# Kernel optimization log

Hardware: AMD Instinct MI355X
Metric: run time of the kernel (lower is better)

The kernel has to match this reference:

```python
import jax, jax.numpy as jnp
import numpy as np

N, E, D, ED = 50000, 800000, 64, 2


def setup_inputs() -> dict:
    key = jax.random.key(0)
    ks = jax.random.split(key, 16)
    inp = {
        "h": jax.random.normal(ks[0], (N, D), jnp.float32),
        "coord": jax.random.normal(ks[1], (N, 3), jnp.float32),
        "edge_index": jax.random.randint(ks[2], (2, E), 0, N, jnp.int32),
        "edge_attr": jax.random.normal(ks[3], (E, ED), jnp.float32),
        # edge_mlp: Linear(2D+1+ED -> D), Linear(D -> D)
        "W_e1": jax.random.normal(ks[4], (2 * D + 1 + ED, D), jnp.float32) * 0.08,
        "b_e1": jnp.zeros((D,), jnp.float32),
        "W_e2": jax.random.normal(ks[5], (D, D), jnp.float32) * 0.12,
        "b_e2": jnp.zeros((D,), jnp.float32),
        # node_mlp: Linear(D+D -> D), Linear(D -> D)
        "W_n1": jax.random.normal(ks[6], (2 * D, D), jnp.float32) * 0.08,
        "b_n1": jnp.zeros((D,), jnp.float32),
        "W_n2": jax.random.normal(ks[7], (D, D), jnp.float32) * 0.12,
        "b_n2": jnp.zeros((D,), jnp.float32),
        # coord_mlp: Linear(D -> D), Linear(D -> 1, bias=False, xavier gain 0.001)
        "W_c1": jax.random.normal(ks[8], (D, D), jnp.float32) * 0.12,
        "b_c1": jnp.zeros((D,), jnp.float32),
        "W_c2": jax.random.normal(ks[9], (D, 1), jnp.float32) * 1e-3,
    }
    return inp


def reference(h, coord, edge_index, edge_attr,
              W_e1, b_e1, W_e2, b_e2,
              W_n1, b_n1, W_n2, b_n2,
              W_c1, b_c1, W_c2):
    row, col = edge_index[0], edge_index[1]
    n_nodes = h.shape[0]

    # coord2radial
    coord_diff = coord[row] - coord[col]                       # [E,3]
    radial = jnp.sum(coord_diff * coord_diff, axis=-1, keepdims=True)  # [E,1]

    # edge_model
    e_in = jnp.concatenate([h[row], h[col], radial, edge_attr], axis=-1)  # [E, 2D+1+ED]
    e = jax.nn.silu(e_in @ W_e1 + b_e1)
    edge_feat = jax.nn.silu(e @ W_e2 + b_e2)                   # [E,D]

    # coord_model: trans = coord_diff * coord_mlp(edge_feat), clamp, segment mean
    scale = jax.nn.silu(edge_feat @ W_c1 + b_c1) @ W_c2        # [E,1]
    trans = jnp.clip(coord_diff * scale, -100.0, 100.0)        # [E,3]
    agg_c = jax.ops.segment_sum(trans, row, num_segments=n_nodes)       # [N,3]
    cnt = jax.ops.segment_sum(jnp.ones((trans.shape[0],), trans.dtype), row,
                              num_segments=n_nodes)            # [N]
    coord_out = coord + agg_c / jnp.clip(cnt, 1.0, None)[:, None]  # coords_weight=1.0

    # node_model: segment sum of edge_feat by row, node MLP, residual
    agg_h = jax.ops.segment_sum(edge_feat, row, num_segments=n_nodes)   # [N,D]
    n_in = jnp.concatenate([h, agg_h], axis=-1)                # [N,2D]
    h_out = h + (jax.nn.silu(n_in @ W_n1 + b_n1) @ W_n2 + b_n2)

    return (h_out, coord_out)
```

## Files before the change

kernel.cpp:

```cpp
#include <hip/hip_runtime.h>

#define DD 64
#define SLOTMAX 64

using s8v   = __attribute__((ext_vector_type(8))) short;
using f32x4 = __attribute__((ext_vector_type(4))) float;

typedef unsigned int   uint_t;
typedef unsigned short ushort_t;

union U8 { s8v v; uint_t u[4]; };

__device__ __forceinline__ float silu_f(float x) {
    return x / (1.0f + __expf(-x));
}
__device__ __forceinline__ float clamp100(float x) {
    return fminf(fmaxf(x, -100.0f), 100.0f);
}
__device__ __forceinline__ unsigned short f2bf(float x) {
    unsigned int u = __float_as_uint(x);
    return (unsigned short)((u + 0x7FFFu + ((u >> 16) & 1u)) >> 16);
}
__device__ __forceinline__ float bf2f(ushort_t v) {
    return __uint_as_float(((uint_t)v) << 16);
}
__device__ __forceinline__ uint_t cvt_pk_bf16(float lo, float hi) {
    uint_t r;
    asm("v_cvt_pk_bf16_f32 %0, %1, %2" : "=v"(r) : "v"(lo), "v"(hi));
    return r;
}

#define WAVE_FENCE() do { asm volatile("s_waitcnt lgkmcnt(0)" ::: "memory"); \
                          __builtin_amdgcn_sched_barrier(0); } while (0)

__global__ __launch_bounds__(256) void prep_all(
    const float* __restrict__ h,
    const float* __restrict__ coord,
    const float* __restrict__ We1, const float* __restrict__ We2,
    const float* __restrict__ Wc1,
    const float* __restrict__ Wn1, const float* __restrict__ Wn2,
    const float* __restrict__ be1, const float* __restrict__ be2,
    const float* __restrict__ bc1,
    const int*   __restrict__ ei,
    ushort_t* __restrict__ hbf,
    ushort_t* __restrict__ wf,
    float4* __restrict__ coord4,
    int* __restrict__ cnt_i,
    int* __restrict__ slots,
    int N, int E, int total8, int histBlocks, int hbfBlocks, int c4Blocks)
{
    const int b = blockIdx.x;
    if (b < histBlocks) {
        const int e = b * 256 + threadIdx.x;
        if (e < E) {
            const int r = ei[e];
            const int s = atomicAdd(&cnt_i[r], 1);
            if (s < SLOTMAX) slots[(size_t)r * SLOTMAX + s] = e;
        }
    } else if (b < histBlocks + hbfBlocks) {
        const int t = (b - histBlocks) * 256 + threadIdx.x;
        if (t < total8) {
            const float4 v0 = ((const float4*)h)[t * 2 + 0];
            const float4 v1 = ((const float4*)h)[t * 2 + 1];
            uint4 o;
            o.x = (uint_t)f2bf(v0.x) | ((uint_t)f2bf(v0.y) << 16);
            o.y = (uint_t)f2bf(v0.z) | ((uint_t)f2bf(v0.w) << 16);
            o.z = (uint_t)f2bf(v1.x) | ((uint_t)f2bf(v1.y) << 16);
            o.w = (uint_t)f2bf(v1.z) | ((uint_t)f2bf(v1.w) << 16);
            ((uint4*)hbf)[t] = o;
        }
    } else if (b < histBlocks + hbfBlocks + c4Blocks) {
        const int t = (b - histBlocks - hbfBlocks) * 256 + threadIdx.x;
        if (t < N) {
            float4 c;
            c.x = coord[3 * t + 0];
            c.y = coord[3 * t + 1];
            c.z = coord[3 * t + 2];
            c.w = 0.0f;
            coord4[t] = c;
        }
    } else {
        const int t = (b - histBlocks - hbfBlocks - c4Blocks) * 256 + threadIdx.x;
        if (t >= 32768) return;
        if (t < 28672) {
            const int j    = t & 7;
            const int lane = (t >> 3) & 63;
            const int n0   = (t >> 9) & 3;
            const int k0   = (t >> 11) & 1;
            const int mat  = t >> 12;
            const int g    = lane >> 4;
            int k;
            if (mat == 2 || mat == 3) k = 16 * (2 * k0 + (j >> 2)) + 4 * g + (j & 3);
            else                      k = k0 * 32 + g * 8 + j;
            const int n = n0 * 16 + (lane & 15);
            float v;
            if      (mat == 0) v = We1[(size_t)k * 64 + n];
            else if (mat == 1) v = We1[(size_t)(64 + k) * 64 + n];
            else if (mat == 2) v = We2[(size_t)k * 64 + n];
            else if (mat == 3) v = Wc1[(size_t)k * 64 + n];
            else if (mat == 4) v = Wn1[(size_t)k * 64 + n];
            else if (mat == 5) v = Wn1[(size_t)(64 + k) * 64 + n];
            else               v = Wn2[(size_t)k * 64 + n];
            wf[t] = f2bf(v);
        } else {
            const int t2   = t - 28672;
            const int j    = t2 & 7;
            const int lane = (t2 >> 3) & 63;
            const int n0   = (t2 >> 9) & 3;
            const int xm   = (t2 >> 11) & 1;
            const int k = 8 * (lane >> 4) + j;
            const int m = n0 * 16 + (lane & 15);
            float v = 0.0f;
            if (xm == 0) {
                if      (k == 0) v = We1[(size_t)128 * 64 + m];
                else if (k == 1) v = We1[(size_t)129 * 64 + m];
                else if (k == 2) v = We1[(size_t)130 * 64 + m];
                else if (k == 3) v = be1[m];
            } else {
                if      (k == 0) v = be2[m];
                else if (k == 1) v = bc1[m];
            }
            wf[t] = f2bf(v);
        }
    }
}

__global__ __launch_bounds__(512, 4) void egcl_edge(
    const ushort_t* __restrict__ hbf,
    const ushort_t* __restrict__ wfG,
    const float4* __restrict__ coord4,
    const int*   __restrict__ ei,
    const float* __restrict__ ea,
    const float* __restrict__ Wc2,
    uint_t* __restrict__ efu,
    float4* __restrict__ trans4,
    int E, int ntiles, int totalWaves)
{
    __shared__ ushort_t fragLDS[20480];

    const int tid = threadIdx.x;
    #pragma unroll
    for (int i = 0; i < 4; ++i)
        ((uint4*)fragLDS)[tid + i * 512] = ((const uint4*)wfG)[tid + i * 512];
    ((uint4*)fragLDS)[2048 + tid] = ((const uint4*)wfG)[3584 + tid];
    __syncthreads();

    const int wid  = tid >> 6;
    const int lane = tid & 63;
    const int l15  = lane & 15;
    const int g    = lane >> 4;

#define LD_W(mat, k0, m0) \
    (*(const s8v*)(fragLDS + ((((mat)*2 + (k0))*4 + (m0)) * 512) + lane * 8))
#define LD_X7(m0) (*(const s8v*)(fragLDS + 16384 + (m0) * 512 + lane * 8))
#define LD_XB(m0) (*(const s8v*)(fragLDS + 18432 + (m0) * 512 + lane * 8))

    float wc2_c[4][4];
    #pragma unroll
    for (int m0 = 0; m0 < 4; ++m0)
        #pragma unroll
        for (int j = 0; j < 4; ++j)
            wc2_c[m0][j] = Wc2[m0 * 16 + 4 * g + j];

    U8 b2f, bcf;
    b2f.u[0] = 0x00003F80u; b2f.u[1] = 0; b2f.u[2] = 0; b2f.u[3] = 0;
    bcf.u[0] = 0x3F800000u; bcf.u[1] = 0; bcf.u[2] = 0; bcf.u[3] = 0;

    const f32x4 zero4 = {0.f, 0.f, 0.f, 0.f};

    for (int t = blockIdx.x * 8 + wid; t < ntiles; t += totalWaves) {
        const int e   = t * 16 + l15;
        const bool val = (e < E);
        const int eL  = val ? e : (E - 1);

        const int row = ei[eL];
        const int col = ei[E + eL];
        const float4 cr = coord4[row];
        const float4 cc = coord4[col];
        const float2 a2 = *(const float2*)(ea + 2 * (size_t)eL);
        const ushort_t* hr = hbf + (size_t)row * 64;
        const ushort_t* hc = hbf + (size_t)col * 64;
        const s8v br0 = *(const s8v*)(hr + g * 8);
        const s8v br1 = *(const s8v*)(hr + 32 + g * 8);
        const s8v bc0 = *(const s8v*)(hc + g * 8);
        const s8v bc1 = *(const s8v*)(hc + 32 + g * 8);

        const float dx = cr.x - cc.x, dy = cr.y - cc.y, dz = cr.z - cc.z;
        const float radial = dx * dx + dy * dy + dz * dz;

        U8 ex;
        ex.u[0] = cvt_pk_bf16(radial, a2.x);
        ex.u[1] = cvt_pk_bf16(a2.y, 1.0f);
        ex.u[2] = 0; ex.u[3] = 0;

        f32x4 c1[4];
        #pragma unroll
        for (int m0 = 0; m0 < 4; ++m0) {
            f32x4 a = zero4;
            a = __builtin_amdgcn_mfma_f32_16x16x32_bf16(LD_W(0, 0, m0), br0, a, 0, 0, 0);
            a = __builtin_amdgcn_mfma_f32_16x16x32_bf16(LD_W(0, 1, m0), br1, a, 0, 0, 0);
            a = __builtin_amdgcn_mfma_f32_16x16x32_bf16(LD_W(1, 0, m0), bc0, a, 0, 0, 0);
            a = __builtin_amdgcn_mfma_f32_16x16x32_bf16(LD_W(1, 1, m0), bc1, a, 0, 0, 0);
            a = __builtin_amdgcn_mfma_f32_16x16x32_bf16(LD_X7(m0),      ex.v, a, 0, 0, 0);
            c1[m0] = a;
        }

        U8 f2a, f2b;
        #pragma unroll
        for (int m0 = 0; m0 < 4; ++m0) {
            const float ya = silu_f(c1[m0][0]);
            const float yb = silu_f(c1[m0][1]);
            const float yc = silu_f(c1[m0][2]);
            const float yd = silu_f(c1[m0][3]);
            U8& dst = (m0 < 2) ? f2a : f2b;
            dst.u[(m0 & 1) * 2 + 0] = cvt_pk_bf16(ya, yb);
            dst.u[(m0 & 1) * 2 + 1] = cvt_pk_bf16(yc, yd);
        }

        f32x4 c2[4];
        #pragma unroll
        for (int m0 = 0; m0 < 4; ++m0) {
            f32x4 a = zero4;
            a = __builtin_amdgcn_mfma_f32_16x16x32_bf16(LD_W(2, 0, m0), f2a.v, a, 0, 0, 0);
            a = __builtin_amdgcn_mfma_f32_16x16x32_bf16(LD_W(2, 1, m0), f2b.v, a, 0, 0, 0);
            a = __builtin_amdgcn_mfma_f32_16x16x32_bf16(LD_XB(m0),      b2f.v, a, 0, 0, 0);
            c2[m0] = a;
        }

        uint_t* efrow = efu + (size_t)e * 32;
        U8 f3a, f3b;
        #pragma unroll
        for (int m0 = 0; m0 < 4; ++m0) {
            const float ya = silu_f(c2[m0][0]);
            const float yb = silu_f(c2[m0][1]);
            const float yc = silu_f(c2[m0][2]);
            const float yd = silu_f(c2[m0][3]);
            const uint_t p0 = cvt_pk_bf16(ya, yb);
            const uint_t p1 = cvt_pk_bf16(yc, yd);
            U8& dst = (m0 < 2) ? f3a : f3b;
            dst.u[(m0 & 1) * 2 + 0] = p0;
            dst.u[(m0 & 1) * 2 + 1] = p1;
            if (val) {
                uint2 st; st.x = p0; st.y = p1;
                *(uint2*)(efrow + m0 * 8 + g * 2) = st;
            }
        }

        float p = 0.f;
        #pragma unroll
        for (int m0 = 0; m0 < 4; ++m0) {
            f32x4 a = zero4;
            a = __builtin_amdgcn_mfma_f32_16x16x32_bf16(LD_W(3, 0, m0), f3a.v, a, 0, 0, 0);
            a = __builtin_amdgcn_mfma_f32_16x16x32_bf16(LD_W(3, 1, m0), f3b.v, a, 0, 0, 0);
            a = __builtin_amdgcn_mfma_f32_16x16x32_bf16(LD_XB(m0),      bcf.v, a, 0, 0, 0);
            #pragma unroll
            for (int j = 0; j < 4; ++j)
                p = fmaf(silu_f(a[j]), wc2_c[m0][j], p);
        }
        p += __shfl_xor(p, 16, 64);
        p += __shfl_xor(p, 32, 64);

        if (val && g == 0) {
            float4 tr;
            tr.x = clamp100(dx * p);
            tr.y = clamp100(dy * p);
            tr.z = clamp100(dz * p);
            tr.w = 1.0f;
            trans4[e] = tr;
        }
    }
#undef LD_W
#undef LD_X7
#undef LD_XB
}

__global__ __launch_bounds__(256) void egcl_agg(
    const ushort_t* __restrict__ efbf,
    const float4* __restrict__ trans4,
    const int* __restrict__ slots,
    const int* __restrict__ cnt_i,
    const float4* __restrict__ coord4,
    ushort_t* __restrict__ aggbf,
    float* __restrict__ coord_out,
    int N)
{
    const int wid  = threadIdx.x >> 6;
    const int lane = threadIdx.x & 63;
    const int n = blockIdx.x * 4 + wid;
    if (n >= N) return;

    const int deg = cnt_i[n];
    const int eff = deg < SLOTMAX ? deg : SLOTMAX;
    const int* sp = slots + (size_t)n * SLOTMAX;

    float a0 = 0.f, a1 = 0.f, a2 = 0.f, a3 = 0.f;
    float tx = 0.f, ty = 0.f, tz = 0.f;

    int s = 0;
    for (; s + 4 <= eff; s += 4) {
        const int e0 = sp[s], e1 = sp[s + 1], e2 = sp[s + 2], e3 = sp[s + 3];
        const float4 t0 = trans4[e0], t1 = trans4[e1], t2 = trans4[e2], t3 = trans4[e3];
        const ushort_t v0 = efbf[(size_t)e0 * 64 + lane];
        const ushort_t v1 = efbf[(size_t)e1 * 64 + lane];
        const ushort_t v2 = efbf[(size_t)e2 * 64 + lane];
        const ushort_t v3 = efbf[(size_t)e3 * 64 + lane];
        a0 += bf2f(v0); a1 += bf2f(v1); a2 += bf2f(v2); a3 += bf2f(v3);
        tx += t0.x + t1.x + t2.x + t3.x;
        ty += t0.y + t1.y + t2.y + t3.y;
        tz += t0.z + t1.z + t2.z + t3.z;
    }
    for (; s < eff; ++s) {
        const int e0 = sp[s];
        a0 += bf2f(efbf[(size_t)e0 * 64 + lane]);
        const float4 t0 = trans4[e0];
        tx += t0.x; ty += t0.y; tz += t0.z;
    }

    aggbf[(size_t)n * 64 + lane] = f2bf(a0 + a1 + a2 + a3);
    if (lane == 0) {
        const float inv = 1.0f / fmaxf((float)deg, 1.0f);
        const float4 cn = coord4[n];
        coord_out[(size_t)n * 3 + 0] = cn.x + tx * inv;
        coord_out[(size_t)n * 3 + 1] = cn.y + ty * inv;
        coord_out[(size_t)n * 3 + 2] = cn.z + tz * inv;
    }
}

__global__ __launch_bounds__(512, 4) void egcl_node(
    const ushort_t* __restrict__ hbf,
    const ushort_t* __restrict__ aggbf,
    const ushort_t* __restrict__ wfG,
    const float* __restrict__ h,
    const float* __restrict__ bn1,
    const float* __restrict__ bn2,
    float* __restrict__ h_out,
    int N)
{
    __shared__ ushort_t fragLDS[12288];
    __shared__ ushort_t ldsY[8][16 * 72];

    const int tid = threadIdx.x;
    #pragma unroll
    for (int i = 0; i < 3; ++i)
        ((uint4*)fragLDS)[tid + i * 512] = ((const uint4*)(wfG + 16384))[tid + i * 512];
    __syncthreads();

    const int wid  = tid >> 6;
    const int lane = tid & 63;
    const int l15  = lane & 15;
    const int g    = lane >> 4;

#define LD_WN(mat, k0, n0) \
    (*(const s8v*)(fragLDS + ((((mat)*2 + (k0))*4 + (n0)) * 512) + lane * 8))

    float bn1_c[4], bn2_c[4];
    #pragma unroll
    for (int n0 = 0; n0 < 4; ++n0) {
        bn1_c[n0] = bn1[n0 * 16 + l15];
        bn2_c[n0] = bn2[n0 * 16 + l15];
    }

    const int wg = blockIdx.x * 8 + wid;
    const int nb = wg * 16;
    if (nb >= N) return;

    const int nod  = nb + l15;
    const int nodL = nod < N ? nod : N - 1;
    const ushort_t* hrow = hbf   + (size_t)nodL * 64;
    const ushort_t* arow = aggbf + (size_t)nodL * 64;
    const s8v aH0 = *(const s8v*)(hrow + g * 8);
    const s8v aH1 = *(const s8v*)(hrow + 32 + g * 8);
    const s8v aG0 = *(const s8v*)(arow + g * 8);
    const s8v aG1 = *(const s8v*)(arow + 32 + g * 8);

    ushort_t* yw = ldsY[wid];
    #pragma unroll
    for (int n0 = 0; n0 < 4; ++n0) {
        f32x4 a = {0.f, 0.f, 0.f, 0.f};
        a = __builtin_amdgcn_mfma_f32_16x16x32_bf16(aH0, LD_WN(0, 0, n0), a, 0, 0, 0);
        a = __builtin_amdgcn_mfma_f32_16x16x32_bf16(aH1, LD_WN(0, 1, n0), a, 0, 0, 0);
        a = __builtin_amdgcn_mfma_f32_16x16x32_bf16(aG0, LD_WN(1, 0, n0), a, 0, 0, 0);
        a = __builtin_amdgcn_mfma_f32_16x16x32_bf16(aG1, LD_WN(1, 1, n0), a, 0, 0, 0);
        #pragma unroll
        for (int jj = 0; jj < 4; ++jj)
            yw[(g * 4 + jj) * 72 + n0 * 16 + l15] = f2bf(silu_f(a[jj] + bn1_c[n0]));
    }
    WAVE_FENCE();

    const ushort_t* yrow = yw + l15 * 72;
    const s8v b0 = *(const s8v*)(yrow + g * 8);
    const s8v b1 = *(const s8v*)(yrow + 32 + g * 8);
    #pragma unroll
    for (int n0 = 0; n0 < 4; ++n0) {
        f32x4 a = {0.f, 0.f, 0.f, 0.f};
        a = __builtin_amdgcn_mfma_f32_16x16x32_bf16(b0, LD_WN(2, 0, n0), a, 0, 0, 0);
        a = __builtin_amdgcn_mfma_f32_16x16x32_bf16(b1, LD_WN(2, 1, n0), a, 0, 0, 0);
        #pragma unroll
        for (int jj = 0; jj < 4; ++jj) {
            const int m = nb + g * 4 + jj;
            if (m < N) {
                const size_t idx = (size_t)m * 64 + n0 * 16 + l15;
                h_out[idx] = h[idx] + (a[jj] + bn2_c[n0]);
            }
        }
    }
#undef LD_WN
}

extern "C" void kernel_launch(void* const* d_in, const int* in_sizes, int n_in,
                              void* d_out, int out_size, void* d_ws, size_t ws_size,
                              hipStream_t stream) {
    const float* h     = (const float*)d_in[0];
    const float* coord = (const float*)d_in[1];
    const int*   ei    = (const int*)  d_in[2];
    const float* ea    = (const float*)d_in[3];
    const float* We1   = (const float*)d_in[4];
    const float* be1   = (const float*)d_in[5];
    const float* We2   = (const float*)d_in[6];
    const float* be2   = (const float*)d_in[7];
    const float* Wn1   = (const float*)d_in[8];
    const float* bn1   = (const float*)d_in[9];
    const float* Wn2   = (const float*)d_in[10];
    const float* bn2   = (const float*)d_in[11];
    const float* Wc1   = (const float*)d_in[12];
    const float* bc1   = (const float*)d_in[13];
    const float* Wc2   = (const float*)d_in[14];

    const int N = in_sizes[0] / DD;
    const int E = in_sizes[3] / 2;

    float* out       = (float*)d_out;
    float* h_out     = out;
    float* coord_out = out + (size_t)N * DD;

    char* base = (char*)d_ws;
    ushort_t* hbf   = (ushort_t*)base;
    const size_t o_wf    = (size_t)N * DD * 2;
    ushort_t* wf    = (ushort_t*)(base + o_wf);
    const size_t o_agg   = o_wf + 32768 * 2;
    ushort_t* aggbf = (ushort_t*)(base + o_agg);
    const size_t o_c4    = o_agg + (size_t)N * DD * 2;
    float4* coord4  = (float4*)(base + o_c4);
    const size_t o_cnt   = o_c4 + (size_t)N * 16;
    int* cnt_i      = (int*)(base + o_cnt);
    const size_t o_slots = o_cnt + (size_t)N * 4;
    int* slots      = (int*)(base + o_slots);
    const size_t o_tr    = o_slots + (size_t)N * SLOTMAX * 4;
    float4* trans4  = (float4*)(base + o_tr);
    const size_t o_ef    = o_tr + (size_t)E * 16;
    ushort_t* efbf  = (ushort_t*)(base + o_ef);

    hipMemsetAsync((void*)cnt_i, 0, (size_t)N * 4, stream);

    const int histBlocks = (E + 255) / 256;
    const int total8     = N * DD / 8;
    const int hbfBlocks  = (total8 + 255) / 256;
    const int c4Blocks   = (N + 255) / 256;
    const int wfBlocks   = (32768 + 255) / 256;
    prep_all<<<histBlocks + hbfBlocks + c4Blocks + wfBlocks, 256, 0, stream>>>(
        h, coord, We1, We2, Wc1, Wn1, Wn2, be1, be2, bc1, ei,
        hbf, wf, coord4, cnt_i, slots, N, E, total8,
        histBlocks, hbfBlocks, c4Blocks);

    const int ntiles = (E + 15) / 16;
    const int eblocks = 1024;
    const int totalWaves = eblocks * 8;
    egcl_edge<<<eblocks, 512, 0, stream>>>(
        hbf, wf, coord4, ei, ea, Wc2,
        (uint_t*)efbf, trans4, E, ntiles, totalWaves);

    const int ablocks = (N + 3) / 4;
    egcl_agg<<<ablocks, 256, 0, stream>>>(
        efbf, trans4, slots, cnt_i, coord4, aggbf, coord_out, N);

    const int nwaves  = (N + 15) / 16;
    const int nblocks = (nwaves + 7) / 8;
    egcl_node<<<nblocks, 512, 0, stream>>>(
        hbf, aggbf, wf, h, bn1, bn2, h_out, N);
}
```

Before: 218.8 us.

## Sort edges by destination row into CSR order so aggregation reads contiguously

Replaces the per-node slot lists with a CSR-style permutation. A scan kernel computes per-node start offsets and a fill kernel writes packed (row, col, bf16 edge_attr) records in row-grouped order. The edge kernel reads these packed records and writes edge features and trans in permuted order, so the aggregation kernel reads each node's edges as contiguous vectorized rows instead of scattered 128-byte gathers. In exchange it adds two extra launches and a second atomic pass over the edges, and block order from the atomic cursor makes the edge order nondeterministic.

After: 227.3 us. +3.9%, slower.

```diff
diff --git a/kernel.cpp b/kernel.cpp
--- a/kernel.cpp
+++ b/kernel.cpp
@@ -46,17 +46,12 @@
     ushort_t* __restrict__ wf,
     float4* __restrict__ coord4,
     int* __restrict__ cnt_i,
-    int* __restrict__ slots,
     int N, int E, int total8, int histBlocks, int hbfBlocks, int c4Blocks)
 {
     const int b = blockIdx.x;
     if (b < histBlocks) {
         const int e = b * 256 + threadIdx.x;
-        if (e < E) {
-            const int r = ei[e];
-            const int s = atomicAdd(&cnt_i[r], 1);
-            if (s < SLOTMAX) slots[(size_t)r * SLOTMAX + s] = e;
-        }
+        if (e < E) atomicAdd(&cnt_i[ei[e]], 1);
     } else if (b < histBlocks + hbfBlocks) {
         const int t = (b - histBlocks) * 256 + threadIdx.x;
         if (t < total8) {
@@ -125,16 +120,62 @@
     }
 }
 
+__global__ __launch_bounds__(256) void prep_scan(
+    const int* __restrict__ cnt_i,
+    int* __restrict__ cursor,
+    int* __restrict__ nstart,
+    int N)
+{
+    __shared__ int sdata[256];
+    __shared__ int sbase;
+    const int tid = threadIdx.x;
+    const int n = blockIdx.x * 256 + tid;
+    int deg = 0;
+    if (n < N) { deg = cnt_i[n]; if (deg > SLOTMAX) deg = SLOTMAX; }
+    sdata[tid] = deg;
+    __syncthreads();
+    for (int off = 1; off < 256; off <<= 1) {
+        const int t = (tid >= off) ? sdata[tid - off] : 0;
+        __syncthreads();
+        sdata[tid] += t;
+        __syncthreads();
+    }
+    if (tid == 255) sbase = atomicAdd(cursor, sdata[255]);
+    __syncthreads();
+    if (n < N) nstart[n] = sbase + sdata[tid] - deg;
+}
+
+__global__ __launch_bounds__(256) void prep_fill(
+    const int* __restrict__ ei,
+    const float* __restrict__ ea,
+    const int* __restrict__ nstart,
+    int* __restrict__ cnt2,
+    int4* __restrict__ eperm4,
+    int E)
+{
+    const int e = blockIdx.x * 256 + threadIdx.x;
+    if (e >= E) return;
+    const int r = ei[e];
+    const int s = atomicAdd(&cnt2[r], 1);
+    if (s < SLOTMAX) {
+        const int c = ei[E + e];
+        const float2 a2 = *(const float2*)(ea + 2 * (size_t)e);
+        const uint_t pk = cvt_pk_bf16(a2.x, a2.y);
+        int4 v; v.x = r; v.y = c; v.z = (int)pk; v.w = 0;
+        eperm4[(size_t)nstart[r] + s] = v;
+    }
+}
+
 __global__ __launch_bounds__(512, 4) void egcl_edge(
     const ushort_t* __restrict__ hbf,
     const ushort_t* __restrict__ wfG,
     const float4* __restrict__ coord4,
-    const int*   __restrict__ ei,
-    const float* __restrict__ ea,
+    const int4* __restrict__ eperm4,
+    const int* __restrict__ cursorP,
     const float* __restrict__ Wc2,
     uint_t* __restrict__ efu,
     float4* __restrict__ trans4,
-    int E, int ntiles, int totalWaves)
+    int totalWaves)
 {
     __shared__ ushort_t fragLDS[20480];
 
@@ -145,6 +186,7 @@
     ((uint4*)fragLDS)[2048 + tid] = ((const uint4*)wfG)[3584 + tid];
     __syncthreads();
 
+    const int P = cursorP[0];
     const int wid  = tid >> 6;
     const int lane = tid & 63;
     const int l15  = lane & 15;
@@ -168,16 +210,18 @@
 
     const f32x4 zero4 = {0.f, 0.f, 0.f, 0.f};
 
-    for (int t = blockIdx.x * 8 + wid; t < ntiles; t += totalWaves) {
-        const int e   = t * 16 + l15;
-        const bool val = (e < E);
-        const int eL  = val ? e : (E - 1);
-
-        const int row = ei[eL];
-        const int col = ei[E + eL];
+    for (int t = blockIdx.x * 8 + wid; t * 16 < P; t += totalWaves) {
+        const int p   = t * 16 + l15;
+        const bool val = (p < P);
+        const int pL  = val ? p : (P - 1);
+
+        const int4 e4 = eperm4[pL];
+        const int row = e4.x;
+        const int col = e4.y;
+        const uint_t eap = (uint_t)e4.z;
+
         const float4 cr = coord4[row];
         const float4 cc = coord4[col];
-        const float2 a2 = *(const float2*)(ea + 2 * (size_t)eL);
         const ushort_t* hr = hbf + (size_t)row * 64;
         const ushort_t* hc = hbf + (size_t)col * 64;
         const s8v br0 = *(const s8v*)(hr + g * 8);
@@ -189,8 +233,9 @@
         const float radial = dx * dx + dy * dy + dz * dz;
 
         U8 ex;
-        ex.u[0] = cvt_pk_bf16(radial, a2.x);
-        ex.u[1] = cvt_pk_bf16(a2.y, 1.0f);
+        const float ea0f = __uint_as_float(eap << 16);
+        ex.u[0] = cvt_pk_bf16(radial, ea0f);
+        ex.u[1] = (eap >> 16) | 0x3F800000u;
         ex.u[2] = 0; ex.u[3] = 0;
 
         f32x4 c1[4];
@@ -227,7 +272,7 @@
             c2[m0] = a;
         }
 
-        uint_t* efrow = efu + (size_t)e * 32;
+        uint_t* efrow = efu + (size_t)pL * 32;
         U8 f3a, f3b;
         #pragma unroll
         for (int m0 = 0; m0 < 4; ++m0) {
@@ -246,7 +291,7 @@
             }
         }
 
-        float p = 0.f;
+        float pacc = 0.f;
         #pragma unroll
         for (int m0 = 0; m0 < 4; ++m0) {
             f32x4 a = zero4;
@@ -255,18 +300,18 @@
             a = __builtin_amdgcn_mfma_f32_16x16x32_bf16(LD_XB(m0),      bcf.v, a, 0, 0, 0);
             #pragma unroll
             for (int j = 0; j < 4; ++j)
-                p = fmaf(silu_f(a[j]), wc2_c[m0][j], p);
-        }
-        p += __shfl_xor(p, 16, 64);
-        p += __shfl_xor(p, 32, 64);
+                pacc = fmaf(silu_f(a[j]), wc2_c[m0][j], pacc);
+        }
+        pacc += __shfl_xor(pacc, 16, 64);
+        pacc += __shfl_xor(pacc, 32, 64);
 
         if (val && g == 0) {
             float4 tr;
-            tr.x = clamp100(dx * p);
-            tr.y = clamp100(dy * p);
-            tr.z = clamp100(dz * p);
-            tr.w = 1.0f;
-            trans4[e] = tr;
+            tr.x = clamp100(dx * pacc);
+            tr.y = clamp100(dy * pacc);
+            tr.z = clamp100(dz * pacc);
+            tr.w = 0.0f;
+            trans4[p] = tr;
         }
     }
 #undef LD_W
@@ -277,7 +322,7 @@
 __global__ __launch_bounds__(256) void egcl_agg(
     const ushort_t* __restrict__ efbf,
     const float4* __restrict__ trans4,
-    const int* __restrict__ slots,
+    const int* __restrict__ nstart,
     const int* __restrict__ cnt_i,
     const float4* __restrict__ coord4,
     ushort_t* __restrict__ aggbf,
@@ -291,32 +336,41 @@
 
     const int deg = cnt_i[n];
     const int eff = deg < SLOTMAX ? deg : SLOTMAX;
-    const int* sp = slots + (size_t)n * SLOTMAX;
-
-    float a0 = 0.f, a1 = 0.f, a2 = 0.f, a3 = 0.f;
+    const int p0  = nstart[n];
+
+    const int sub = lane >> 4;
+    const int dp  = lane & 15;
+
+    float ax = 0.f, ay = 0.f, az = 0.f, aw = 0.f;
+    for (int s = sub; s < eff; s += 4) {
+        const uint2 v = *(const uint2*)(efbf + (size_t)(p0 + s) * 64 + dp * 4);
+        ax += __uint_as_float(v.x << 16);
+        ay += __uint_as_float(v.x & 0xFFFF0000u);
+        az += __uint_as_float(v.y << 16);
+        aw += __uint_as_float(v.y & 0xFFFF0000u);
+    }
+    ax += __shfl_xor(ax, 16, 64); ay += __shfl_xor(ay, 16, 64);
+    az += __shfl_xor(az, 16, 64); aw += __shfl_xor(aw, 16, 64);
+    ax += __shfl_xor(ax, 32, 64); ay += __shfl_xor(ay, 32, 64);
+    az += __shfl_xor(az, 32, 64); aw += __shfl_xor(aw, 32, 64);
+    if (sub == 0) {
+        uint2 st;
+        st.x = cvt_pk_bf16(ax, ay);
+        st.y = cvt_pk_bf16(az, aw);
+        *(uint2*)(aggbf + (size_t)n * 64 + dp * 4) = st;
+    }
+
     float tx = 0.f, ty = 0.f, tz = 0.f;
-
-    int s = 0;
-    for (; s + 4 <= eff; s += 4) {
-        const int e0 = sp[s], e1 = sp[s + 1], e2 = sp[s + 2], e3 = sp[s + 3];
-        const float4 t0 = trans4[e0], t1 = trans4[e1], t2 = trans4[e2], t3 = trans4[e3];
-        const ushort_t v0 = efbf[(size_t)e0 * 64 + lane];
-        const ushort_t v1 = efbf[(size_t)e1 * 64 + lane];
-        const ushort_t v2 = efbf[(size_t)e2 * 64 + lane];
-        const ushort_t v3 = efbf[(size_t)e3 * 64 + lane];
-        a0 += bf2f(v0); a1 += bf2f(v1); a2 += bf2f(v2); a3 += bf2f(v3);
-        tx += t0.x + t1.x + t2.x + t3.x;
-        ty += t0.y + t1.y + t2.y + t3.y;
-        tz += t0.z + t1.z + t2.z + t3.z;
-    }
-    for (; s < eff; ++s) {
-        const int e0 = sp[s];
-        a0 += bf2f(efbf[(size_t)e0 * 64 + lane]);
-        const float4 t0 = trans4[e0];
-        tx += t0.x; ty += t0.y; tz += t0.z;
-    }
-
-    aggbf[(size_t)n * 64 + lane] = f2bf(a0 + a1 + a2 + a3);
+    for (int s = lane; s < eff; s += 64) {
+        const float4 tr = trans4[p0 + s];
+        tx += tr.x; ty += tr.y; tz += tr.z;
+    }
+    #pragma unroll
+    for (int msk = 1; msk < 64; msk <<= 1) {
+        tx += __shfl_xor(tx, msk, 64);
+        ty += __shfl_xor(ty, msk, 64);
+        tz += __shfl_xor(tz, msk, 64);
+    }
     if (lane == 0) {
         const float inv = 1.0f / fmaxf((float)deg, 1.0f);
         const float4 cn = coord4[n];
@@ -443,14 +497,17 @@
     float4* coord4  = (float4*)(base + o_c4);
     const size_t o_cnt   = o_c4 + (size_t)N * 16;
     int* cnt_i      = (int*)(base + o_cnt);
-    const size_t o_slots = o_cnt + (size_t)N * 4;
-    int* slots      = (int*)(base + o_slots);
-    const size_t o_tr    = o_slots + (size_t)N * SLOTMAX * 4;
+    int* cnt2       = cnt_i + N;
+    int* cursor     = cnt_i + 2 * N;
+    int* nstart     = cnt_i + 2 * N + 4;
+    const size_t o_ep    = o_cnt + ((size_t)3 * N + 4) * 4 + 8;
+    int4* eperm4    = (int4*)(base + ((o_ep + 15) & ~(size_t)15));
+    const size_t o_tr    = ((o_ep + 15) & ~(size_t)15) + (size_t)E * 16;
     float4* trans4  = (float4*)(base + o_tr);
     const size_t o_ef    = o_tr + (size_t)E * 16;
     ushort_t* efbf  = (ushort_t*)(base + o_ef);
 
-    hipMemsetAsync((void*)cnt_i, 0, (size_t)N * 4, stream);
+    hipMemsetAsync((void*)cnt_i, 0, ((size_t)2 * N + 4) * 4, stream);
 
     const int histBlocks = (E + 255) / 256;
     const int total8     = N * DD / 8;
@@ -459,19 +516,22 @@
     const int wfBlocks   = (32768 + 255) / 256;
     prep_all<<<histBlocks + hbfBlocks + c4Blocks + wfBlocks, 256, 0, stream>>>(
         h, coord, We1, We2, Wc1, Wn1, Wn2, be1, be2, bc1, ei,
-        hbf, wf, coord4, cnt_i, slots, N, E, total8,
+        hbf, wf, coord4, cnt_i, N, E, total8,
         histBlocks, hbfBlocks, c4Blocks);
 
-    const int ntiles = (E + 15) / 16;
+    prep_scan<<<(N + 255) / 256, 256, 0, stream>>>(cnt_i, cursor, nstart, N);
+
+    prep_fill<<<(E + 255) / 256, 256, 0, stream>>>(ei, ea, nstart, cnt2, eperm4, E);
+
     const int eblocks = 1024;
     const int totalWaves = eblocks * 8;
     egcl_edge<<<eblocks, 512, 0, stream>>>(
-        hbf, wf, coord4, ei, ea, Wc2,
-        (uint_t*)efbf, trans4, E, ntiles, totalWaves);
+        hbf, wf, coord4, eperm4, cursor, Wc2,
+        (uint_t*)efbf, trans4, totalWaves);
 
     const int ablocks = (N + 3) / 4;
     egcl_agg<<<ablocks, 256, 0, stream>>>(
-        efbf, trans4, slots, cnt_i, coord4, aggbf, coord_out, N);
+        efbf, trans4, nstart, cnt_i, coord4, aggbf, coord_out, N);
 
     const int nwaves  = (N + 15) / 16;
     const int nblocks = (nwaves + 7) / 8;
```

## Use atomic work-stealing tile counter in edge kernel and unroll aggregation by eight

Applied to the files above, without the earlier changes.

The edge kernel stops striding tiles statically by wave and instead has each wave grab its next tile from a global atomic counter, fetching the following index ahead so the atomic's latency overlaps the current tile. This is meant to balance load across waves that finish unevenly. The counter sits right after the degree counts and is zeroed by the same memset. Separately, the aggregation loop is unrolled to eight edges with all loads issued before accumulating, to put more gathers in flight; one atomic per tile across about 50k tiles adds global contention.

Result: slower. 808.1 us (+269.3%).

```diff
diff --git a/kernel.cpp b/kernel.cpp
--- a/kernel.cpp
+++ b/kernel.cpp
@@ -134,7 +134,8 @@
     const float* __restrict__ Wc2,
     uint_t* __restrict__ efu,
     float4* __restrict__ trans4,
-    int E, int ntiles, int totalWaves)
+    int* __restrict__ tileCtr,
+    int E, int ntiles)
 {
     __shared__ ushort_t fragLDS[20480];
 
@@ -145,7 +146,6 @@
     ((uint4*)fragLDS)[2048 + tid] = ((const uint4*)wfG)[3584 + tid];
     __syncthreads();
 
-    const int wid  = tid >> 6;
     const int lane = tid & 63;
     const int l15  = lane & 15;
     const int g    = lane >> 4;
@@ -168,7 +168,17 @@
 
     const f32x4 zero4 = {0.f, 0.f, 0.f, 0.f};
 
-    for (int t = blockIdx.x * 8 + wid; t < ntiles; t += totalWaves) {
+    int t;
+    {
+        int t0 = 0;
+        if (lane == 0) t0 = atomicAdd(tileCtr, 1);
+        t = __shfl(t0, 0, 64);
+    }
+
+    while (t < ntiles) {
+        int nt0 = 0;
+        if (lane == 0) nt0 = atomicAdd(tileCtr, 1);
+
         const int e   = t * 16 + l15;
         const bool val = (e < E);
         const int eL  = val ? e : (E - 1);
@@ -268,6 +278,8 @@
             tr.w = 1.0f;
             trans4[e] = tr;
         }
+
+        t = __shfl(nt0, 0, 64);
     }
 #undef LD_W
 #undef LD_X7
@@ -293,30 +305,35 @@
     const int eff = deg < SLOTMAX ? deg : SLOTMAX;
     const int* sp = slots + (size_t)n * SLOTMAX;
 
-    float a0 = 0.f, a1 = 0.f, a2 = 0.f, a3 = 0.f;
+    float acc = 0.f;
     float tx = 0.f, ty = 0.f, tz = 0.f;
 
     int s = 0;
-    for (; s + 4 <= eff; s += 4) {
-        const int e0 = sp[s], e1 = sp[s + 1], e2 = sp[s + 2], e3 = sp[s + 3];
-        const float4 t0 = trans4[e0], t1 = trans4[e1], t2 = trans4[e2], t3 = trans4[e3];
-        const ushort_t v0 = efbf[(size_t)e0 * 64 + lane];
-        const ushort_t v1 = efbf[(size_t)e1 * 64 + lane];
-        const ushort_t v2 = efbf[(size_t)e2 * 64 + lane];
-        const ushort_t v3 = efbf[(size_t)e3 * 64 + lane];
-        a0 += bf2f(v0); a1 += bf2f(v1); a2 += bf2f(v2); a3 += bf2f(v3);
-        tx += t0.x + t1.x + t2.x + t3.x;
-        ty += t0.y + t1.y + t2.y + t3.y;
-        tz += t0.z + t1.z + t2.z + t3.z;
+    for (; s + 8 <= eff; s += 8) {
+        int e_[8];
+        #pragma unroll
+        for (int u = 0; u < 8; ++u) e_[u] = sp[s + u];
+        float v_[8];
+        float4 t_[8];
+        #pragma unroll
+        for (int u = 0; u < 8; ++u) {
+            v_[u] = bf2f(efbf[(size_t)e_[u] * 64 + lane]);
+            t_[u] = trans4[e_[u]];
+        }
+        #pragma unroll
+        for (int u = 0; u < 8; ++u) {
+            acc += v_[u];
+            tx += t_[u].x; ty += t_[u].y; tz += t_[u].z;
+        }
     }
     for (; s < eff; ++s) {
         const int e0 = sp[s];
-        a0 += bf2f(efbf[(size_t)e0 * 64 + lane]);
+        acc += bf2f(efbf[(size_t)e0 * 64 + lane]);
         const float4 t0 = trans4[e0];
         tx += t0.x; ty += t0.y; tz += t0.z;
     }
 
-    aggbf[(size_t)n * 64 + lane] = f2bf(a0 + a1 + a2 + a3);
+    aggbf[(size_t)n * 64 + lane] = f2bf(acc);
     if (lane == 0) {
         const float inv = 1.0f / fmaxf((float)deg, 1.0f);
         const float4 cn = coord4[n];
@@ -443,14 +460,15 @@
     float4* coord4  = (float4*)(base + o_c4);
     const size_t o_cnt   = o_c4 + (size_t)N * 16;
     int* cnt_i      = (int*)(base + o_cnt);
-    const size_t o_slots = o_cnt + (size_t)N * 4;
+    int* tileCtr    = cnt_i + N;
+    const size_t o_slots = o_cnt + ((size_t)N + 4) * 4;
     int* slots      = (int*)(base + o_slots);
     const size_t o_tr    = o_slots + (size_t)N * SLOTMAX * 4;
     float4* trans4  = (float4*)(base + o_tr);
     const size_t o_ef    = o_tr + (size_t)E * 16;
     ushort_t* efbf  = (ushort_t*)(base + o_ef);
 
-    hipMemsetAsync((void*)cnt_i, 0, (size_t)N * 4, stream);
+    hipMemsetAsync((void*)cnt_i, 0, ((size_t)N + 4) * 4, stream);
 
     const int histBlocks = (E + 255) / 256;
     const int total8     = N * DD / 8;
@@ -464,10 +482,9 @@
 
     const int ntiles = (E + 15) / 16;
     const int eblocks = 1024;
-    const int totalWaves = eblocks * 8;
     egcl_edge<<<eblocks, 512, 0, stream>>>(
         hbf, wf, coord4, ei, ea, Wc2,
-        (uint_t*)efbf, trans4, E, ntiles, totalWaves);
+        (uint_t*)efbf, trans4, tileCtr, E, ntiles);
 
     const int ablocks = (N + 3) / 4;
     egcl_agg<<<ablocks, 256, 0, stream>>>(
```
